# Optimization experiments

Hardware: AMD Instinct MI355X
Metric: run time of the kernel (lower is better)

Reference implementation:

```python
import jax, jax.numpy as jnp
import numpy as np

LEAK_VALUE = 0.1
B, N_ATOMS, IN_F, H, MAX_VAL, OUT_F = 256, 128, 128, 256, 6, 256


def gru(x, W_ih, W_hh, b_ih, b_hh):
    # x: [B, T, in]; W_ih: [3H, in]; W_hh: [3H, H]; gate order r,z,n (torch)
    Bb, T, _ = x.shape
    Hh = W_hh.shape[1]
    x_proj = jnp.einsum('bti,gi->btg', x, W_ih) + b_ih  # [B, T, 3H]

    def step(h, xp):
        gh = h @ W_hh.T + b_hh                      # [B, 3H]
        xr, xz, xn = jnp.split(xp, 3, axis=-1)
        hr, hz, hn = jnp.split(gh, 3, axis=-1)
        r = jax.nn.sigmoid(xr + hr)
        z = jax.nn.sigmoid(xz + hz)
        n = jnp.tanh(xn + r * hn)
        h_new = (1.0 - z) * n + z * h
        return h_new, h_new

    h0 = jnp.zeros((Bb, Hh), x.dtype)
    _, out = jax.lax.scan(step, h0, jnp.swapaxes(x_proj, 0, 1))  # [T, B, H]
    return jnp.swapaxes(out, 0, 1)  # [B, T, H]


def setup_inputs() -> dict:
    key = jax.random.key(0)
    ks = jax.random.split(key, 8)
    s = 0.05
    return {
        'x': jax.random.normal(ks[0], (B, N_ATOMS, IN_F), jnp.float32),
        'bonded_atoms': jax.random.randint(ks[1], (B, N_ATOMS, MAX_VAL), 0, N_ATOMS),
        'W_ih': jax.random.normal(ks[2], (3 * H, IN_F), jnp.float32) * s,
        'W_hh': jax.random.normal(ks[3], (3 * H, H), jnp.float32) * s,
        'b_ih': jax.random.normal(ks[4], (3 * H,), jnp.float32) * s,
        'b_hh': jax.random.normal(ks[5], (3 * H,), jnp.float32) * s,
        'W_fc': jax.random.normal(ks[6], (OUT_F, H * MAX_VAL), jnp.float32) * s,
        'b_fc': jax.random.normal(ks[7], (OUT_F,), jnp.float32) * s,
    }


def reference(x, bonded_atoms, W_ih, W_hh, b_ih, b_hh, W_fc, b_fc):
    rnn_out = gru(x, W_ih, W_hh, b_ih, b_hh)               # [B, N, H]
    batch_idx = jnp.arange(x.shape[0])[:, None, None]       # [B, 1, 1]
    fc_in = rnn_out[batch_idx, bonded_atoms]                # [B, N, V, H] gather
    fc_in = fc_in.reshape(x.shape[0], x.shape[1], -1)       # [B, N, V*H]
    out = fc_in @ W_fc.T + b_fc                             # [B, N, OUT_F]
    return jnp.where(out >= 0, out, LEAK_VALUE * out)
```

## Files before the change

### kernel.cpp

```cpp
#include <hip/hip_runtime.h>
#include <hip/hip_bf16.h>
#include <stdint.h>

typedef unsigned short u16;
typedef __bf16 bf16_t;
typedef bf16_t bf16x8 __attribute__((ext_vector_type(8)));
typedef u16    u16x8  __attribute__((ext_vector_type(8)));
typedef u16    u16x4  __attribute__((ext_vector_type(4)));
typedef float  f32x4  __attribute__((ext_vector_type(4)));

#define BSZ    256
#define NATOMS 128
#define INF    128
#define HH     256
#define H3     768
#define MAXV   6
#define OUTF   256
#define KFC    (HH * MAXV)
#define PLANE  8388608
#define HAP    264

__device__ __forceinline__ u16 f2bf(float f) {
  union { float f; unsigned u; } v; v.f = f;
  unsigned u = v.u;
  unsigned r = (u + 0x7FFFu + ((u >> 16) & 1u)) >> 16;
  return (u16)r;
}
__device__ __forceinline__ float bf2f(u16 h) {
  union { unsigned u; float f; } v; v.u = ((unsigned)h) << 16;
  return v.f;
}
__device__ __forceinline__ f32x4 mfma_bf16(u16x8 a, u16x8 b, f32x4 c) {
  return __builtin_amdgcn_mfma_f32_16x16x32_bf16(
      __builtin_bit_cast(bf16x8, a), __builtin_bit_cast(bf16x8, b), c, 0, 0, 0);
}
__device__ __forceinline__ float sel4(float a0, float a1, float a2, float a3, int q) {
  float t01 = (q & 1) ? a1 : a0;
  float t23 = (q & 1) ? a3 : a2;
  return (q & 2) ? t23 : t01;
}

#define NX4   1048576
#define C1    1048576
#define C2    1073152
#define C3    1122304
#define C4    1220608
__global__ void k_prep4(const float* __restrict__ x, const float* __restrict__ wih,
                        const float* __restrict__ whh, const float* __restrict__ wfc,
                        u16* __restrict__ xb, u16* __restrict__ wihb,
                        u16* __restrict__ whhb, u16* __restrict__ wfcb) {
  int i = blockIdx.x * 256 + threadIdx.x;
  const float* src; u16* dst; int j;
  if (i < C1)      { src = x;   dst = xb;   j = i; }
  else if (i < C2) { src = wih; dst = wihb; j = i - C1; }
  else if (i < C3) { src = whh; dst = whhb; j = i - C2; }
  else             { src = wfc; dst = wfcb; j = i - C3; }
  f32x4 v = *(const f32x4*)(src + (size_t)j * 4);
  u16x4 o;
#pragma unroll
  for (int k = 0; k < 4; k++) o[k] = f2bf(v[k]);
  *(u16x4*)(dst + (size_t)j * 4) = o;
}

__global__ __launch_bounds__(256) void k_xproj(const u16* __restrict__ X,
                                               const u16* __restrict__ W,
                                               const float* __restrict__ bias,
                                               const float* __restrict__ bhh,
                                               u16* __restrict__ out) {
  __shared__ __align__(16) u16 As[128][136];
  __shared__ __align__(16) u16 Bs[128][136];
  const int tid = threadIdx.x, lane = tid & 63, wid = tid >> 6;
  const int c16 = lane & 15, quad = lane >> 4;
  const int wm = (wid & 1) * 64, wn = (wid >> 1) * 64;
  const int bg = blockIdx.x >> 2, tg = blockIdx.x & 3;
  const int n0 = blockIdx.y * 128;

#pragma unroll
  for (int j = 0; j < 8; j++) {
    const int u = tid + j * 256, row = u >> 4, ch = u & 15;
    const int b = bg * 4 + (row & 3), t = tg * 32 + (row >> 2);
    *(u16x8*)&As[row][ch * 8] =
        *(const u16x8*)(X + ((size_t)b * 16384 + t * 128 + ch * 8));
    *(u16x8*)&Bs[row][ch * 8] =
        *(const u16x8*)(W + ((size_t)(n0 + row) * 128 + ch * 8));
  }
  __syncthreads();

  const f32x4 zero = {0.f, 0.f, 0.f, 0.f};
  f32x4 acc[4][4];
#pragma unroll
  for (int mi = 0; mi < 4; mi++)
#pragma unroll
    for (int ni = 0; ni < 4; ni++) acc[mi][ni] = zero;

#pragma unroll
  for (int kt = 0; kt < 4; kt++) {
    u16x8 af[4], bf[4];
#pragma unroll
    for (int mi = 0; mi < 4; mi++)
      af[mi] = *(const u16x8*)&As[wm + mi * 16 + c16][kt * 32 + quad * 8];
#pragma unroll
    for (int ni = 0; ni < 4; ni++)
      bf[ni] = *(const u16x8*)&Bs[wn + ni * 16 + c16][kt * 32 + quad * 8];
#pragma unroll
    for (int mi = 0; mi < 4; mi++)
#pragma unroll
      for (int ni = 0; ni < 4; ni++)
        acc[mi][ni] = mfma_bf16(af[mi], bf[ni], acc[mi][ni]);
  }

  const int bb = bg >> 2, mbh = bg & 3;
#pragma unroll
  for (int ni = 0; ni < 4; ni++) {
    const int n = n0 + wn + ni * 16 + c16;
    const int g = n >> 8, ww = (n >> 5) & 7, pp = (n >> 4) & 1, cc = n & 15;
    const float badd = bias[n] + (g < 2 ? bhh[n] : 0.f);
    u16* plane = out + (size_t)g * PLANE;
#pragma unroll
    for (int mi = 0; mi < 4; mi++) {
      const int t = tg * 32 + (wm >> 2) + mi * 4 + quad;
      u16x4 sv;
#pragma unroll
      for (int r_ = 0; r_ < 4; r_++) sv[r_] = f2bf(acc[mi][ni][r_] + badd);
      *(u16x4*)(plane + (((size_t)((bb * 128 + t) * 8 + ww)) << 9) +
                (mbh * 16 + cc) * 8 + pp * 4) = sv;
    }
  }
}

__global__ void __attribute__((amdgpu_flat_work_group_size(256, 256),
                               amdgpu_waves_per_eu(1, 1)))
k_gru(const u16* __restrict__ Whh, const float* __restrict__ bhh,
      const u16* __restrict__ xp2, u16* __restrict__ rnn) {
  __shared__ __align__(16) u16 hA[2][4 * HAP];
  const int tid = threadIdx.x, lane = tid & 63, w = tid >> 6;
  const int c = lane & 15, q = lane >> 4;
  const int b0 = blockIdx.x * 4;
  const int bb = blockIdx.x >> 2;
  const int Lq = (blockIdx.x & 3) * 16 + c;

  for (int i = tid; i < 2 * 4 * HAP; i += 256) ((u16*)hA)[i] = 0;

  u16x8 wf[12][8];
#pragma unroll
  for (int nt = 0; nt < 12; nt++)
#pragma unroll
    for (int kt = 0; kt < 8; kt++) {
      const int n = (nt >> 2) * 256 + w * 64 + (nt & 3) * 16 + c;
      wf[nt][kt] = *(const u16x8*)(Whh + (size_t)n * HH + kt * 32 + q * 8);
    }
#pragma unroll
  for (int nt = 0; nt < 12; nt++)
#pragma unroll
    for (int kt = 0; kt < 8; kt++) asm volatile("" : "+a"(wf[nt][kt]));

  const int col = w * 64 + q * 16 + c;
  const float bhhn = bhh[512 + col];
  float hreg[4] = {0.f, 0.f, 0.f, 0.f};

  const u16* gbase = xp2 + ((size_t)(bb * 128) * 8 + (w * 2 + (q >> 1))) * 512 +
                     (size_t)Lq * 8 + (q & 1) * 4;
  const int sl = lane & 31;
  u16* rnn_base = rnn + ((size_t)(b0 + w) * NATOMS) * HH + sl * 8;

  u16x4 xg0[3], xg1[3];
#pragma unroll
  for (int g = 0; g < 3; g++) xg0[g] = *(const u16x4*)(gbase + (size_t)g * PLANE);
#pragma unroll
  for (int g = 0; g < 3; g++) xg1[g] = *(const u16x4*)(gbase + 4096 + (size_t)g * PLANE);
  const u16* gpre = gbase + 2 * 4096;

  asm volatile("s_waitcnt lgkmcnt(0)\n\ts_barrier" ::: "memory");

  const f32x4 zero4 = {0.f, 0.f, 0.f, 0.f};

  auto step = [&](const int t, u16x4 (&xgc)[3]) {
    const u16* hc = hA[t & 1];
    u16* hnx = hA[(t + 1) & 1];

    if (t && lane < 32) {
      const u16x8 hv8 = *(const u16x8*)&hc[w * HAP + sl * 8];
      *(u16x8*)(rnn_base + (size_t)(t - 1) * HH) = hv8;
    }

    u16x4 xg[3];
#pragma unroll
    for (int g = 0; g < 3; g++) xg[g] = xgc[g];
    if (t < NATOMS - 2) {
#pragma unroll
      for (int g = 0; g < 3; g++)
        xgc[g] = *(const u16x4*)(gpre + (size_t)g * PLANE);
    }

    f32x4 acc[12];
    u16x8 a0 = *(const u16x8*)&hc[(c & 3) * HAP + q * 8];
#pragma unroll
    for (int kt = 0; kt < 8; kt++) {
      u16x8 a1;
      if (kt < 7)
        a1 = *(const u16x8*)&hc[(c & 3) * HAP + (kt + 1) * 32 + q * 8];
      if (kt == 0) {
#pragma unroll
        for (int nt = 0; nt < 12; nt++) acc[nt] = mfma_bf16(a0, wf[nt][0], zero4);
      } else {
#pragma unroll
        for (int nt = 0; nt < 12; nt++) acc[nt] = mfma_bf16(a0, wf[nt][kt], acc[nt]);
      }
      a0 = a1;
    }

#pragma unroll
    for (int r_ = 0; r_ < 4; r_++) {
      const float Ar = sel4(acc[0][r_], acc[1][r_], acc[2][r_], acc[3][r_], q);
      const float Az = sel4(acc[4][r_], acc[5][r_], acc[6][r_], acc[7][r_], q);
      const float An = sel4(acc[8][r_], acc[9][r_], acc[10][r_], acc[11][r_], q);
      const float ar = Ar + bf2f(xg[0][r_]);
      const float az = Az + bf2f(xg[1][r_]);
      const float hn = An + bhhn;
      const float xn = bf2f(xg[2][r_]);
      const float rr = 1.f / (1.f + __expf(-ar));
      const float zz = 1.f / (1.f + __expf(-az));
      const float e  = __expf(2.f * (xn + rr * hn));
      const float nn = 1.f - 2.f / (e + 1.f);
      const float hv = nn + zz * (hreg[r_] - nn);
      hreg[r_] = hv;
      hnx[r_ * HAP + col] = f2bf(hv);
    }

    asm volatile("s_waitcnt lgkmcnt(0)\n\ts_barrier" ::: "memory");
  };

#pragma unroll 1
  for (int tt = 0; tt < NATOMS; tt += 2) {
    step(tt, xg0);
    gpre += 4096;
    step(tt + 1, xg1);
    gpre += 4096;
  }

  if (lane < 32) {
    const u16x8 hv8 = *(const u16x8*)&hA[0][w * HAP + sl * 8];
    *(u16x8*)(rnn_base + (size_t)(NATOMS - 1) * HH) = hv8;
  }
}

__global__ __launch_bounds__(256) void k_fc(const u16* __restrict__ rnn,
                                            const int* __restrict__ bonded,
                                            const u16* __restrict__ W,
                                            const float* __restrict__ bias,
                                            float* __restrict__ out) {
  __shared__ __align__(16) u16 As[128][72];
  __shared__ __align__(16) u16 Bs[128][72];
  __shared__ int ic[128][6];
  const int tid = threadIdx.x, lane = tid & 63, wid = tid >> 6;
  const int c16 = lane & 15, quad = lane >> 4;
  const int wNm = (wid & 1) * 64;
  const int wNa = (wid >> 1) * 64;
  const int bx = blockIdx.x, n0 = blockIdx.y * 128;

  for (int u = tid; u < 768; u += 256) {
    const int v = u >> 7, row = u & 127;
    ic[row][v] = bonded[(size_t)(bx * 128 + row) * MAXV + v];
  }
  __syncthreads();

  const f32x4 zero = {0.f, 0.f, 0.f, 0.f};
  f32x4 acc[4][4];
#pragma unroll
  for (int mi = 0; mi < 4; mi++)
#pragma unroll
    for (int ni = 0; ni < 4; ni++) acc[mi][ni] = zero;

  for (int it = 0; it < 24; it++) {
    const int kk = it * 64, v = kk >> 8, kr = kk & 255;
#pragma unroll
    for (int j = 0; j < 4; j++) {
      const int u = tid + j * 256, row = u >> 3, ch = u & 7;
      const int idx = ic[row][v];
      *(u16x8*)&As[row][ch * 8] =
          *(const u16x8*)(rnn + ((size_t)(bx * 128 + idx)) * HH + kr + ch * 8);
      *(u16x8*)&Bs[row][ch * 8] =
          *(const u16x8*)(W + (size_t)(n0 + row) * KFC + kk + ch * 8);
    }
    __syncthreads();
#pragma unroll
    for (int kt = 0; kt < 2; kt++) {
      u16x8 aw[4], ba[4];
#pragma unroll
      for (int mi = 0; mi < 4; mi++)
        aw[mi] = *(const u16x8*)&Bs[wNm + mi * 16 + c16][kt * 32 + quad * 8];
#pragma unroll
      for (int ni = 0; ni < 4; ni++)
        ba[ni] = *(const u16x8*)&As[wNa + ni * 16 + c16][kt * 32 + quad * 8];
#pragma unroll
      for (int mi = 0; mi < 4; mi++)
#pragma unroll
        for (int ni = 0; ni < 4; ni++)
          acc[mi][ni] = mfma_bf16(aw[mi], ba[ni], acc[mi][ni]);
    }
    __syncthreads();
  }

#pragma unroll
  for (int mi = 0; mi < 4; mi++) {
    const int n = n0 + wNm + mi * 16 + quad * 4;
    const f32x4 bv = *(const f32x4*)(bias + n);
#pragma unroll
    for (int ni = 0; ni < 4; ni++) {
      const int mm = bx * 128 + wNa + ni * 16 + c16;
      f32x4 vv;
#pragma unroll
      for (int r_ = 0; r_ < 4; r_++) {
        const float t = acc[mi][ni][r_] + bv[r_];
        vv[r_] = t >= 0.f ? t : 0.1f * t;
      }
      *(f32x4*)(out + (size_t)mm * OUTF + n) = vv;
    }
  }
}

extern "C" void kernel_launch(void* const* d_in, const int* in_sizes, int n_in,
                              void* d_out, int out_size, void* d_ws, size_t ws_size,
                              hipStream_t stream) {
  const float* x      = (const float*)d_in[0];
  const int*   bonded = (const int*)d_in[1];
  const float* Wih    = (const float*)d_in[2];
  const float* Whh    = (const float*)d_in[3];
  const float* bih    = (const float*)d_in[4];
  const float* bhh    = (const float*)d_in[5];
  const float* Wfc    = (const float*)d_in[6];
  const float* bfc    = (const float*)d_in[7];
  float* out = (float*)d_out;

  char* ws = (char*)d_ws;
  u16* xp2  = (u16*)(ws);
  u16* rnn  = (u16*)(ws + 50331648);
  u16* whhb = (u16*)(ws + 67108864);
  u16* wfcb = (u16*)(ws + 67502080);
  u16* xb   = (u16*)(ws + 68288512);
  u16* wihb = (u16*)(ws + 76677120);

  k_prep4<<<C4 / 256, 256, 0, stream>>>(x, Wih, Whh, Wfc, xb, wihb, whhb, wfcb);
  k_xproj<<<dim3(256, 6), 256, 0, stream>>>(xb, wihb, bih, bhh, xp2);
  k_gru<<<64, 256, 0, stream>>>(whhb, bhh, xp2, rnn);
  k_fc<<<dim3(256, 2), 256, 0, stream>>>(rnn, bonded, wfcb, bfc, out);
}
```

Baseline: 339.0 us.

## Spill part of GRU recurrent weights to LDS and double-buffer FC tile loads

In the GRU kernel, only the first 5 of 8 K-slices of W_hh stay in registers. The last 3 are staged in shared memory and reloaded every step, which lowers register and AGPR pressure at the cost of extra LDS traffic on the serial recurrence path. In the FC kernel, the next K tile is prefetched from global memory into registers while MFMAs run on the current tile, then written into a second LDS buffer. This overlaps the gather and weight loads with compute and needs only one barrier per iteration.

```diff
diff --git a/kernel.cpp b/kernel.cpp
--- a/kernel.cpp
+++ b/kernel.cpp
@@ -133,6 +133,7 @@
 k_gru(const u16* __restrict__ Whh, const float* __restrict__ bhh,
       const u16* __restrict__ xp2, u16* __restrict__ rnn) {
   __shared__ __align__(16) u16 hA[2][4 * HAP];
+  __shared__ __align__(16) u16 wS[4][12][3][512];
   const int tid = threadIdx.x, lane = tid & 63, w = tid >> 6;
   const int c = lane & 15, q = lane >> 4;
   const int b0 = blockIdx.x * 4;
@@ -141,18 +142,27 @@
 
   for (int i = tid; i < 2 * 4 * HAP; i += 256) ((u16*)hA)[i] = 0;
 
-  u16x8 wf[12][8];
+  u16x8 wf[12][5];
 #pragma unroll
   for (int nt = 0; nt < 12; nt++)
 #pragma unroll
-    for (int kt = 0; kt < 8; kt++) {
+    for (int kt = 0; kt < 5; kt++) {
       const int n = (nt >> 2) * 256 + w * 64 + (nt & 3) * 16 + c;
       wf[nt][kt] = *(const u16x8*)(Whh + (size_t)n * HH + kt * 32 + q * 8);
     }
 #pragma unroll
   for (int nt = 0; nt < 12; nt++)
 #pragma unroll
-    for (int kt = 0; kt < 8; kt++) asm volatile("" : "+a"(wf[nt][kt]));
+    for (int kt = 0; kt < 5; kt++) asm volatile("" : "+a"(wf[nt][kt]));
+
+#pragma unroll
+  for (int nt = 0; nt < 12; nt++)
+#pragma unroll
+    for (int kts = 0; kts < 3; kts++) {
+      const int n = (nt >> 2) * 256 + w * 64 + (nt & 3) * 16 + c;
+      *(u16x8*)&wS[w][nt][kts][lane * 8] =
+          *(const u16x8*)(Whh + (size_t)n * HH + (5 + kts) * 32 + q * 8);
+    }
 
   const int col = w * 64 + q * 16 + c;
   const float bhhn = bhh[512 + col];
@@ -202,9 +212,16 @@
       if (kt == 0) {
 #pragma unroll
         for (int nt = 0; nt < 12; nt++) acc[nt] = mfma_bf16(a0, wf[nt][0], zero4);
+      } else if (kt < 5) {
+#pragma unroll
+        for (int nt = 0; nt < 12; nt++) acc[nt] = mfma_bf16(a0, wf[nt][kt], acc[nt]);
       } else {
-#pragma unroll
-        for (int nt = 0; nt < 12; nt++) acc[nt] = mfma_bf16(a0, wf[nt][kt], acc[nt]);
+        u16x8 wb[12];
+#pragma unroll
+        for (int nt = 0; nt < 12; nt++)
+          wb[nt] = *(const u16x8*)&wS[w][nt][kt - 5][lane * 8];
+#pragma unroll
+        for (int nt = 0; nt < 12; nt++) acc[nt] = mfma_bf16(a0, wb[nt], acc[nt]);
       }
       a0 = a1;
     }
@@ -249,14 +266,15 @@
                                             const u16* __restrict__ W,
                                             const float* __restrict__ bias,
                                             float* __restrict__ out) {
-  __shared__ __align__(16) u16 As[128][72];
-  __shared__ __align__(16) u16 Bs[128][72];
+  __shared__ __align__(16) u16 As[2][128][72];
+  __shared__ __align__(16) u16 Bs[2][128][72];
   __shared__ int ic[128][6];
   const int tid = threadIdx.x, lane = tid & 63, wid = tid >> 6;
   const int c16 = lane & 15, quad = lane >> 4;
   const int wNm = (wid & 1) * 64;
   const int wNa = (wid >> 1) * 64;
   const int bx = blockIdx.x, n0 = blockIdx.y * 128;
+  const int srow = tid >> 3, sch = tid & 7;
 
   for (int u = tid; u < 768; u += 256) {
     const int v = u >> 7, row = u & 127;
@@ -264,6 +282,33 @@
   }
   __syncthreads();
 
+  u16x8 ra[4], rb[4];
+#define STAGE_LOAD(IT)                                                         \
+  {                                                                            \
+    const int kk_ = (IT) * 64, v_ = kk_ >> 8, kr_ = kk_ & 255;                 \
+    _Pragma("unroll")                                                          \
+    for (int j = 0; j < 4; j++) {                                              \
+      const int row_ = srow + j * 32;                                          \
+      const int idx_ = ic[row_][v_];                                           \
+      ra[j] = *(const u16x8*)(rnn + ((size_t)(bx * 128 + idx_)) * HH + kr_ +   \
+                              sch * 8);                                        \
+      rb[j] = *(const u16x8*)(W + (size_t)(n0 + row_) * KFC + kk_ + sch * 8);  \
+    }                                                                          \
+  }
+#define STAGE_WRITE(B_)                                                        \
+  {                                                                            \
+    _Pragma("unroll")                                                          \
+    for (int j = 0; j < 4; j++) {                                              \
+      const int row_ = srow + j * 32;                                          \
+      *(u16x8*)&As[B_][row_][sch * 8] = ra[j];                                 \
+      *(u16x8*)&Bs[B_][row_][sch * 8] = rb[j];                                 \
+    }                                                                          \
+  }
+
+  STAGE_LOAD(0);
+  STAGE_WRITE(0);
+  __syncthreads();
+
   const f32x4 zero = {0.f, 0.f, 0.f, 0.f};
   f32x4 acc[4][4];
 #pragma unroll
@@ -271,33 +316,26 @@
 #pragma unroll
     for (int ni = 0; ni < 4; ni++) acc[mi][ni] = zero;
 
+#pragma unroll 1
   for (int it = 0; it < 24; it++) {
-    const int kk = it * 64, v = kk >> 8, kr = kk & 255;
-#pragma unroll
-    for (int j = 0; j < 4; j++) {
-      const int u = tid + j * 256, row = u >> 3, ch = u & 7;
-      const int idx = ic[row][v];
-      *(u16x8*)&As[row][ch * 8] =
-          *(const u16x8*)(rnn + ((size_t)(bx * 128 + idx)) * HH + kr + ch * 8);
-      *(u16x8*)&Bs[row][ch * 8] =
-          *(const u16x8*)(W + (size_t)(n0 + row) * KFC + kk + ch * 8);
-    }
-    __syncthreads();
+    const int cur = it & 1;
+    if (it < 23) STAGE_LOAD(it + 1);
 #pragma unroll
     for (int kt = 0; kt < 2; kt++) {
       u16x8 aw[4], ba[4];
 #pragma unroll
       for (int mi = 0; mi < 4; mi++)
-        aw[mi] = *(const u16x8*)&Bs[wNm + mi * 16 + c16][kt * 32 + quad * 8];
+        aw[mi] = *(const u16x8*)&Bs[cur][wNm + mi * 16 + c16][kt * 32 + quad * 8];
 #pragma unroll
       for (int ni = 0; ni < 4; ni++)
-        ba[ni] = *(const u16x8*)&As[wNa + ni * 16 + c16][kt * 32 + quad * 8];
+        ba[ni] = *(const u16x8*)&As[cur][wNa + ni * 16 + c16][kt * 32 + quad * 8];
 #pragma unroll
       for (int mi = 0; mi < 4; mi++)
 #pragma unroll
         for (int ni = 0; ni < 4; ni++)
           acc[mi][ni] = mfma_bf16(aw[mi], ba[ni], acc[mi][ni]);
     }
+    if (it < 23) STAGE_WRITE(cur ^ 1);
     __syncthreads();
   }
 
```

After: 351.6 us. +3.7%, slower.
